# Kernel tuning notes

Hardware: AMD Instinct MI355X
Metric: run time of the kernel (lower is better)

The kernel has to match this reference:

```python
import jax, jax.numpy as jnp
import numpy as np
from jax import lax

B, T, P, H, O = 64, 96, 256, 128, 24  # batch, seq_len, num_points, hidden_dim, pred_len


def setup_inputs() -> dict:
    key = jax.random.key(0)
    ks = jax.random.split(key, 7)
    s = 1.0 / np.sqrt(H)  # torch LSTM/Linear default init scale
    return {
        "x": jax.random.normal(ks[0], (B, T, P, 1), dtype=jnp.float32),
        "W_ih": jax.random.uniform(ks[1], (P, 4 * H, 1), jnp.float32, -s, s),
        "W_hh": jax.random.uniform(ks[2], (P, 4 * H, H), jnp.float32, -s, s),
        "b_ih": jax.random.uniform(ks[3], (P, 4 * H), jnp.float32, -s, s),
        "b_hh": jax.random.uniform(ks[4], (P, 4 * H), jnp.float32, -s, s),
        "W_fc": jax.random.uniform(ks[5], (P, O, H), jnp.float32, -s, s),
        "b_fc": jax.random.uniform(ks[6], (P, O), jnp.float32, -s, s),
    }


def reference(x, W_ih, W_hh, b_ih, b_hh, W_fc, b_fc):
    # x: [B, T, P, F]; model uses only feature 0
    xs = x[..., 0]  # [B, T, P]
    # input_dim == 1, so input-to-gate contribution is a scaled broadcast of W_ih
    # precompute for all timesteps: [T, B, P, 4H]
    gx = jnp.einsum("btp,pg->tbpg", xs, W_ih[:, :, 0]) + (b_ih + b_hh)

    def step(carry, gxt):
        h, c = carry  # [B, P, H] each
        gates = gxt + jnp.einsum("bph,pgh->bpg", h, W_hh)  # [B, P, 4H]
        i, f, g, o = jnp.split(gates, 4, axis=-1)  # torch gate order i,f,g,o
        i = jax.nn.sigmoid(i)
        f = jax.nn.sigmoid(f)
        g = jnp.tanh(g)
        o = jax.nn.sigmoid(o)
        c = f * c + i * g
        h = o * jnp.tanh(c)
        return (h, c), None

    h0 = jnp.zeros((B, P, H), dtype=x.dtype)
    (h, _), _ = lax.scan(step, (h0, h0), gx)
    # per-point Linear on final hidden state: [B, P, O]
    out = jnp.einsum("bph,poh->bpo", h, W_fc) + b_fc
    # original stacks point outputs on last dim -> [B, pred_len, P]
    return jnp.transpose(out, (0, 2, 1))
```

## Files before the change

kernel.cpp:

```cpp
#include <hip/hip_runtime.h>
#include <hip/hip_bf16.h>

#define Bdim 64
#define Tdim 96
#define Pdim 256
#define Hdim 128
#define Gdim 512
#define Odim 24
#define WROW 132

typedef __bf16 bf16x8 __attribute__((ext_vector_type(8)));
typedef float  f32x16 __attribute__((ext_vector_type(16)));

union BF8 { uint2 u2[2]; unsigned short s[8]; bf16x8 v; };

__device__ __forceinline__ unsigned short f2bf(float f) {
    unsigned int u = __float_as_uint(f);
    u = (u + 0x7FFFu + ((u >> 16) & 1u)) >> 16;
    return (unsigned short)u;
}
__device__ __forceinline__ float bf2f(unsigned short s) {
    return __uint_as_float(((unsigned int)s) << 16);
}
__device__ __forceinline__ float exp2_fast(float x) {
#if __has_builtin(__builtin_amdgcn_exp2f)
    return __builtin_amdgcn_exp2f(x);
#else
    return __expf(x * 0.6931471805599453f);
#endif
}
__device__ __forceinline__ float sigm2(float y) {
    return __builtin_amdgcn_rcpf(1.0f + exp2_fast(-y));
}

__global__ __launch_bounds__(1024, 4)
void lstm_fused(const float* __restrict__ x,
                const float* __restrict__ W_ih,
                const float* __restrict__ W_hh,
                const float* __restrict__ b_ih,
                const float* __restrict__ b_hh,
                const float* __restrict__ W_fc,
                const float* __restrict__ b_fc,
                float* __restrict__ out)
{
    __shared__ unsigned short hl[2][Bdim * WROW];

    const int p   = blockIdx.x;
    const int tid = threadIdx.x;
    const int w   = tid >> 6;
    const int l   = tid & 63;
    const int l31 = l & 31;
    const int hi  = l >> 5;

    const float L1 = 1.4426950408889634f;

    for (int i = tid; i < 2 * Bdim * WROW; i += 1024) ((unsigned short*)hl)[i] = 0;

    bf16x8 afr[9];
    {
        const int rp   = w * 32 + l31;
        const int orow = ((rp & 3) << 7) | (rp >> 2);
        const float sc = ((rp & 3) == 2) ? (2.0f * L1) : L1;
        const float* rowp = W_hh + (size_t)p * Gdim * Hdim + (size_t)orow * Hdim;
        #pragma unroll
        for (int ks = 0; ks < 8; ++ks) {
            int k0 = ks * 16 + hi * 8;
            float4 va = *(const float4*)(rowp + k0);
            float4 vb = *(const float4*)(rowp + k0 + 4);
            BF8 u;
            u.s[0] = f2bf(sc * va.x); u.s[1] = f2bf(sc * va.y);
            u.s[2] = f2bf(sc * va.z); u.s[3] = f2bf(sc * va.w);
            u.s[4] = f2bf(sc * vb.x); u.s[5] = f2bf(sc * vb.y);
            u.s[6] = f2bf(sc * vb.z); u.s[7] = f2bf(sc * vb.w);
            afr[ks] = u.v;
        }
        BF8 u9;
        #pragma unroll
        for (int j = 0; j < 8; ++j) u9.s[j] = 0;
        if (hi == 0) {
            u9.s[0] = f2bf(sc * W_ih[(size_t)p * Gdim + orow]);
            u9.s[1] = f2bf(sc * (b_ih[(size_t)p * Gdim + orow] +
                                 b_hh[(size_t)p * Gdim + orow]));
        }
        afr[8] = u9.v;
    }

    float cre[2][4];
    #pragma unroll
    for (int nt = 0; nt < 2; ++nt)
        #pragma unroll
        for (int q = 0; q < 4; ++q) cre[nt][q] = 0.f;

    const float* xp = x + p;
    float xv0 = xp[(size_t)(l31 * Tdim) * Pdim];
    float xv1 = xp[(size_t)((l31 + 32) * Tdim) * Pdim];

    __syncthreads();

    int cur = 0;
    for (int t = 0; t < Tdim; ++t) {
        float xn0 = 0.f, xn1 = 0.f;
        if (t + 1 < Tdim) {
            xn0 = xp[(size_t)(l31 * Tdim + t + 1) * Pdim];
            xn1 = xp[(size_t)((l31 + 32) * Tdim + t + 1) * Pdim];
        }

        f32x16 acc[2];
        #pragma unroll
        for (int j = 0; j < 16; ++j) { acc[0][j] = 0.f; acc[1][j] = 0.f; }

        const char* hbase = (const char*)hl[cur];
        #pragma unroll
        for (int ks = 0; ks < 8; ++ks) {
            int boff = ks * 32 + hi * 16;
            BF8 b0, b1;
            b0.u2[0] = *(const uint2*)(hbase + l31 * (WROW * 2) + boff);
            b0.u2[1] = *(const uint2*)(hbase + l31 * (WROW * 2) + boff + 8);
            b1.u2[0] = *(const uint2*)(hbase + (l31 + 32) * (WROW * 2) + boff);
            b1.u2[1] = *(const uint2*)(hbase + (l31 + 32) * (WROW * 2) + boff + 8);
            acc[0] = __builtin_amdgcn_mfma_f32_32x32x16_bf16(afr[ks], b0.v, acc[0], 0, 0, 0);
            acc[1] = __builtin_amdgcn_mfma_f32_32x32x16_bf16(afr[ks], b1.v, acc[1], 0, 0, 0);
        }
        {
            BF8 b0, b1;
            #pragma unroll
            for (int j = 0; j < 8; ++j) { b0.s[j] = 0; b1.s[j] = 0; }
            unsigned short onebf = hi ? (unsigned short)0 : (unsigned short)0x3F80;
            b0.s[0] = hi ? (unsigned short)0 : f2bf(xv0);
            b0.s[1] = onebf;
            b1.s[0] = hi ? (unsigned short)0 : f2bf(xv1);
            b1.s[1] = onebf;
            acc[0] = __builtin_amdgcn_mfma_f32_32x32x16_bf16(afr[8], b0.v, acc[0], 0, 0, 0);
            acc[1] = __builtin_amdgcn_mfma_f32_32x32x16_bf16(afr[8], b1.v, acc[1], 0, 0, 0);
        }

        unsigned short* hw = hl[cur ^ 1];
        #pragma unroll
        for (int nt = 0; nt < 2; ++nt) {
            #pragma unroll
            for (int q = 0; q < 4; ++q) {
                float iv = sigm2(acc[nt][4 * q + 0]);
                float fv = sigm2(acc[nt][4 * q + 1]);
                float ug = sigm2(acc[nt][4 * q + 2]);
                float gp = __builtin_fmaf(4.0f * L1, ug, -2.0f * L1);
                float ov = sigm2(acc[nt][4 * q + 3]);
                float c  = __builtin_fmaf(fv, cre[nt][q], iv * gp);
                cre[nt][q] = c;
                float v  = __builtin_amdgcn_rcpf(1.0f + exp2_fast(-c));
                float th = __builtin_fmaf(2.0f, v, -1.0f);
                float hv = ov * th;
                int k = w * 8 + 2 * q + hi;
                int b = l31 + 32 * nt;
                hw[b * WROW + k] = f2bf(hv);
            }
        }

        __syncthreads();
        cur ^= 1;
        xv0 = xn0; xv1 = xn1;
    }

    const float* wfc = W_fc + (size_t)p * Odim * Hdim;
    const float* bfc = b_fc + (size_t)p * Odim;
    const unsigned short* hf = hl[cur];
    for (int i = tid; i < Bdim * Odim; i += 1024) {
        int o = i % Odim;
        int b = i / Odim;
        float s = bfc[o];
        const float* wr = wfc + o * Hdim;
        const unsigned short* hr = hf + b * WROW;
        #pragma unroll 8
        for (int k2 = 0; k2 < Hdim; ++k2)
            s = __builtin_fmaf(wr[k2], bf2f(hr[k2]), s);
        out[(size_t)b * Odim * Pdim + (size_t)o * Pdim + p] = s;
    }
}

extern "C" void kernel_launch(void* const* d_in, const int* in_sizes, int n_in,
                              void* d_out, int out_size, void* d_ws, size_t ws_size,
                              hipStream_t stream) {
    const float* x    = (const float*)d_in[0];
    const float* W_ih = (const float*)d_in[1];
    const float* W_hh = (const float*)d_in[2];
    const float* b_ih = (const float*)d_in[3];
    const float* b_hh = (const float*)d_in[4];
    const float* W_fc = (const float*)d_in[5];
    const float* b_fc = (const float*)d_in[6];
    float* out = (float*)d_out;

    lstm_fused<<<dim3(Pdim), dim3(1024), 0, stream>>>(x, W_ih, W_hh, b_ih, b_hh, W_fc, b_fc, out);
}
```

Before: 400.9 us.

## Split batch across two blocks per point, switch to fp16 MFMA, fuse gate math

Each point is now handled by two 512-thread blocks, each owning half the batch. Every wave holds two M-tiles of W_hh and shares one B fragment between them, which halves the LDS reads per MFMA and doubles the grid to 512 blocks. The bf16 MFMA becomes fp16, and the gate nonlinearities are rewritten to share one reciprocal per cell update, with the cell state clamped to ±60. The cost is that W_hh is loaded twice per point (once per block), the register footprint per thread grows, and fp16 has a narrower range than bf16.

```diff
diff --git a/kernel.cpp b/kernel.cpp
--- a/kernel.cpp
+++ b/kernel.cpp
@@ -7,21 +7,15 @@
 #define Hdim 128
 #define Gdim 512
 #define Odim 24
+#define BH   32
 #define WROW 132
 
-typedef __bf16 bf16x8 __attribute__((ext_vector_type(8)));
-typedef float  f32x16 __attribute__((ext_vector_type(16)));
+typedef _Float16 f16x8 __attribute__((ext_vector_type(8)));
+typedef float    f32x16 __attribute__((ext_vector_type(16)));
 
-union BF8 { uint2 u2[2]; unsigned short s[8]; bf16x8 v; };
+union H8 { uint2 u2[2]; unsigned short s[8]; _Float16 h[8]; f16x8 v; };
+union HS { _Float16 h; unsigned short s; };
 
-__device__ __forceinline__ unsigned short f2bf(float f) {
-    unsigned int u = __float_as_uint(f);
-    u = (u + 0x7FFFu + ((u >> 16) & 1u)) >> 16;
-    return (unsigned short)u;
-}
-__device__ __forceinline__ float bf2f(unsigned short s) {
-    return __uint_as_float(((unsigned int)s) << 16);
-}
 __device__ __forceinline__ float exp2_fast(float x) {
 #if __has_builtin(__builtin_amdgcn_exp2f)
     return __builtin_amdgcn_exp2f(x);
@@ -29,11 +23,8 @@
     return __expf(x * 0.6931471805599453f);
 #endif
 }
-__device__ __forceinline__ float sigm2(float y) {
-    return __builtin_amdgcn_rcpf(1.0f + exp2_fast(-y));
-}
 
-__global__ __launch_bounds__(1024, 4)
+__global__ __launch_bounds__(512, 4)
 void lstm_fused(const float* __restrict__ x,
                 const float* __restrict__ W_ih,
                 const float* __restrict__ W_hh,
@@ -43,67 +34,65 @@
                 const float* __restrict__ b_fc,
                 float* __restrict__ out)
 {
-    __shared__ unsigned short hl[2][Bdim * WROW];
+    __shared__ unsigned short hl[2][BH * WROW];
 
-    const int p   = blockIdx.x;
-    const int tid = threadIdx.x;
-    const int w   = tid >> 6;
-    const int l   = tid & 63;
-    const int l31 = l & 31;
-    const int hi  = l >> 5;
+    const int p    = blockIdx.x >> 1;
+    const int half = blockIdx.x & 1;
+    const int tid  = threadIdx.x;
+    const int w    = tid >> 6;
+    const int l    = tid & 63;
+    const int l31  = l & 31;
+    const int hi   = l >> 5;
 
     const float L1 = 1.4426950408889634f;
+    const float L2 = 2.0f * L1;
 
-    for (int i = tid; i < 2 * Bdim * WROW; i += 1024) ((unsigned short*)hl)[i] = 0;
+    for (int i = tid; i < 2 * BH * WROW; i += 512) ((unsigned short*)hl)[i] = 0;
 
-    bf16x8 afr[9];
-    {
-        const int rp   = w * 32 + l31;
+    f16x8 afr[2][9];
+    #pragma unroll
+    for (int mt = 0; mt < 2; ++mt) {
+        const int rp   = w * 64 + mt * 32 + l31;
         const int orow = ((rp & 3) << 7) | (rp >> 2);
-        const float sc = ((rp & 3) == 2) ? (2.0f * L1) : L1;
+        const float sc = ((rp & 3) == 2) ? L2 : L1;
         const float* rowp = W_hh + (size_t)p * Gdim * Hdim + (size_t)orow * Hdim;
         #pragma unroll
         for (int ks = 0; ks < 8; ++ks) {
             int k0 = ks * 16 + hi * 8;
             float4 va = *(const float4*)(rowp + k0);
             float4 vb = *(const float4*)(rowp + k0 + 4);
-            BF8 u;
-            u.s[0] = f2bf(sc * va.x); u.s[1] = f2bf(sc * va.y);
-            u.s[2] = f2bf(sc * va.z); u.s[3] = f2bf(sc * va.w);
-            u.s[4] = f2bf(sc * vb.x); u.s[5] = f2bf(sc * vb.y);
-            u.s[6] = f2bf(sc * vb.z); u.s[7] = f2bf(sc * vb.w);
-            afr[ks] = u.v;
+            H8 u;
+            u.h[0] = (_Float16)(sc * va.x); u.h[1] = (_Float16)(sc * va.y);
+            u.h[2] = (_Float16)(sc * va.z); u.h[3] = (_Float16)(sc * va.w);
+            u.h[4] = (_Float16)(sc * vb.x); u.h[5] = (_Float16)(sc * vb.y);
+            u.h[6] = (_Float16)(sc * vb.z); u.h[7] = (_Float16)(sc * vb.w);
+            afr[mt][ks] = u.v;
         }
-        BF8 u9;
+        H8 u9;
         #pragma unroll
         for (int j = 0; j < 8; ++j) u9.s[j] = 0;
         if (hi == 0) {
-            u9.s[0] = f2bf(sc * W_ih[(size_t)p * Gdim + orow]);
-            u9.s[1] = f2bf(sc * (b_ih[(size_t)p * Gdim + orow] +
-                                 b_hh[(size_t)p * Gdim + orow]));
+            u9.h[0] = (_Float16)(sc * W_ih[(size_t)p * Gdim + orow]);
+            u9.h[1] = (_Float16)(sc * (b_ih[(size_t)p * Gdim + orow] +
+                                       b_hh[(size_t)p * Gdim + orow]));
         }
-        afr[8] = u9.v;
+        afr[mt][8] = u9.v;
     }
 
     float cre[2][4];
     #pragma unroll
-    for (int nt = 0; nt < 2; ++nt)
+    for (int mt = 0; mt < 2; ++mt)
         #pragma unroll
-        for (int q = 0; q < 4; ++q) cre[nt][q] = 0.f;
+        for (int q = 0; q < 4; ++q) cre[mt][q] = 0.f;
 
-    const float* xp = x + p;
-    float xv0 = xp[(size_t)(l31 * Tdim) * Pdim];
-    float xv1 = xp[(size_t)((l31 + 32) * Tdim) * Pdim];
+    const float* xp = x + (size_t)((half * BH + l31) * Tdim) * Pdim + p;
+    float xv = xp[0];
 
     __syncthreads();
 
     int cur = 0;
     for (int t = 0; t < Tdim; ++t) {
-        float xn0 = 0.f, xn1 = 0.f;
-        if (t + 1 < Tdim) {
-            xn0 = xp[(size_t)(l31 * Tdim + t + 1) * Pdim];
-            xn1 = xp[(size_t)((l31 + 32) * Tdim + t + 1) * Pdim];
-        }
+        float xn = (t + 1 < Tdim) ? xp[(size_t)(t + 1) * Pdim] : 0.f;
 
         f32x16 acc[2];
         #pragma unroll
@@ -112,67 +101,76 @@
         const char* hbase = (const char*)hl[cur];
         #pragma unroll
         for (int ks = 0; ks < 8; ++ks) {
-            int boff = ks * 32 + hi * 16;
-            BF8 b0, b1;
-            b0.u2[0] = *(const uint2*)(hbase + l31 * (WROW * 2) + boff);
-            b0.u2[1] = *(const uint2*)(hbase + l31 * (WROW * 2) + boff + 8);
-            b1.u2[0] = *(const uint2*)(hbase + (l31 + 32) * (WROW * 2) + boff);
-            b1.u2[1] = *(const uint2*)(hbase + (l31 + 32) * (WROW * 2) + boff + 8);
-            acc[0] = __builtin_amdgcn_mfma_f32_32x32x16_bf16(afr[ks], b0.v, acc[0], 0, 0, 0);
-            acc[1] = __builtin_amdgcn_mfma_f32_32x32x16_bf16(afr[ks], b1.v, acc[1], 0, 0, 0);
+            int boff = l31 * (WROW * 2) + ks * 32 + hi * 16;
+            H8 b0;
+            b0.u2[0] = *(const uint2*)(hbase + boff);
+            b0.u2[1] = *(const uint2*)(hbase + boff + 8);
+            acc[0] = __builtin_amdgcn_mfma_f32_32x32x16_f16(afr[0][ks], b0.v, acc[0], 0, 0, 0);
+            acc[1] = __builtin_amdgcn_mfma_f32_32x32x16_f16(afr[1][ks], b0.v, acc[1], 0, 0, 0);
         }
         {
-            BF8 b0, b1;
+            H8 b0;
             #pragma unroll
-            for (int j = 0; j < 8; ++j) { b0.s[j] = 0; b1.s[j] = 0; }
-            unsigned short onebf = hi ? (unsigned short)0 : (unsigned short)0x3F80;
-            b0.s[0] = hi ? (unsigned short)0 : f2bf(xv0);
-            b0.s[1] = onebf;
-            b1.s[0] = hi ? (unsigned short)0 : f2bf(xv1);
-            b1.s[1] = onebf;
-            acc[0] = __builtin_amdgcn_mfma_f32_32x32x16_bf16(afr[8], b0.v, acc[0], 0, 0, 0);
-            acc[1] = __builtin_amdgcn_mfma_f32_32x32x16_bf16(afr[8], b1.v, acc[1], 0, 0, 0);
+            for (int j = 0; j < 8; ++j) b0.s[j] = 0;
+            if (hi == 0) { b0.h[0] = (_Float16)xv; b0.h[1] = (_Float16)1.0f; }
+            acc[0] = __builtin_amdgcn_mfma_f32_32x32x16_f16(afr[0][8], b0.v, acc[0], 0, 0, 0);
+            acc[1] = __builtin_amdgcn_mfma_f32_32x32x16_f16(afr[1][8], b0.v, acc[1], 0, 0, 0);
         }
 
         unsigned short* hw = hl[cur ^ 1];
         #pragma unroll
-        for (int nt = 0; nt < 2; ++nt) {
+        for (int mt = 0; mt < 2; ++mt) {
             #pragma unroll
             for (int q = 0; q < 4; ++q) {
-                float iv = sigm2(acc[nt][4 * q + 0]);
-                float fv = sigm2(acc[nt][4 * q + 1]);
-                float ug = sigm2(acc[nt][4 * q + 2]);
-                float gp = __builtin_fmaf(4.0f * L1, ug, -2.0f * L1);
-                float ov = sigm2(acc[nt][4 * q + 3]);
-                float c  = __builtin_fmaf(fv, cre[nt][q], iv * gp);
-                cre[nt][q] = c;
-                float v  = __builtin_amdgcn_rcpf(1.0f + exp2_fast(-c));
-                float th = __builtin_fmaf(2.0f, v, -1.0f);
-                float hv = ov * th;
-                int k = w * 8 + 2 * q + hi;
-                int b = l31 + 32 * nt;
-                hw[b * WROW + k] = f2bf(hv);
+                float yi = acc[mt][4 * q + 0];
+                float yf = acc[mt][4 * q + 1];
+                float yg = acc[mt][4 * q + 2];
+                float yo = acc[mt][4 * q + 3];
+                float Ef = exp2_fast(-yf);
+                float Ei = exp2_fast(-yi);
+                float Eg = exp2_fast(yg);
+                float t1 = 1.0f + Ef;
+                float t2 = 1.0f + Ei;
+                float t3 = Eg + 1.0f;
+                float t4 = Eg - 1.0f;
+                float den = (t1 * t2) * t3;
+                float ct2 = cre[mt][q] * t2;
+                float g4  = L2 * t4;
+                float num = __builtin_fmaf(ct2, t3, g4 * t1);
+                float cn  = num * __builtin_amdgcn_rcpf(den);
+                cn = fminf(60.0f, fmaxf(-60.0f, cn));
+                cre[mt][q] = cn;
+                float Eo = exp2_fast(-yo);
+                float Ec = exp2_fast(cn);
+                float den2 = (1.0f + Eo) * (Ec + 1.0f);
+                float hv = (Ec - 1.0f) * __builtin_amdgcn_rcpf(den2);
+                HS hs; hs.h = (_Float16)hv;
+                int k = w * 16 + mt * 8 + 2 * q + hi;
+                hw[l31 * WROW + k] = hs.s;
             }
         }
 
         __syncthreads();
         cur ^= 1;
-        xv0 = xn0; xv1 = xn1;
+        xv = xn;
     }
 
     const float* wfc = W_fc + (size_t)p * Odim * Hdim;
     const float* bfc = b_fc + (size_t)p * Odim;
     const unsigned short* hf = hl[cur];
-    for (int i = tid; i < Bdim * Odim; i += 1024) {
+    for (int i = tid; i < BH * Odim; i += 512) {
         int o = i % Odim;
         int b = i / Odim;
         float s = bfc[o];
         const float* wr = wfc + o * Hdim;
         const unsigned short* hr = hf + b * WROW;
         #pragma unroll 8
-        for (int k2 = 0; k2 < Hdim; ++k2)
-            s = __builtin_fmaf(wr[k2], bf2f(hr[k2]), s);
-        out[(size_t)b * Odim * Pdim + (size_t)o * Pdim + p] = s;
+        for (int k2 = 0; k2 < Hdim; ++k2) {
+            HS hs; hs.s = hr[k2];
+            s = __builtin_fmaf(wr[k2], (float)hs.h, s);
+        }
+        int bg = half * BH + b;
+        out[(size_t)bg * Odim * Pdim + (size_t)o * Pdim + p] = s;
     }
 }
 
@@ -188,5 +186,5 @@
     const float* b_fc = (const float*)d_in[6];
     float* out = (float*)d_out;
 
-    lstm_fused<<<dim3(Pdim), dim3(1024), 0, stream>>>(x, W_ih, W_hh, b_ih, b_hh, W_fc, b_fc, out);
+    lstm_fused<<<dim3(2 * Pdim), dim3(512), 0, stream>>>(x, W_ih, W_hh, b_ih, b_hh, W_fc, b_fc, out);
 }
```

New measurement: 419.3 us. +4.6%, slower.
